# Performance work log

Hardware: AMD Instinct MI355X
Metric: run time of the kernel (lower is better)

## Reference

```python
import jax, jax.numpy as jnp
import numpy as np

B, N, D = 4, 1024, 1024
H, DH = 16, 64            # heads, dim_head; inner_dim = H*DH = D
CTX_N, CTX_D = 77, 768    # CLIP text context
FF_IN, FF_HID = 8 * D, 4 * D  # GEGLU: proj to 2*4*D, gate to 4*D
EPS = 1e-5
SCALE = DH ** -0.5
NL = 256                  # 2**8 levels for all quantizers
ZP_QKV = 128.0            # asymmetric 8-bit zero point for q/k/v
ZP_W = 0.0                # always_zero=True for softmax-weight quantizer


def _round_ste(t):
    return t + jax.lax.stop_gradient(jnp.round(t) - t)


def _fake_quant(x, delta, zp):
    xq = jnp.clip(_round_ste(x / delta) + zp, 0.0, NL - 1.0)
    return (xq - zp) * delta


def _ln(x, w, b):
    m = x.mean(-1, keepdims=True)
    v = x.var(-1, keepdims=True)
    return (x - m) * jax.lax.rsqrt(v + EPS) * w + b


def _split_heads(t):  # [b, n, h*d] -> [b, h, n, d]
    b, n, _ = t.shape
    return t.reshape(b, n, H, DH).transpose(0, 2, 1, 3)


def _attn(x, ctx, wq, wk, wv, wo, bo, dq, dk, dv, dw):
    q = _split_heads(x @ wq)
    k = _split_heads(ctx @ wk)
    v = _split_heads(ctx @ wv)
    qq = _fake_quant(q, dq, ZP_QKV)
    kk = _fake_quant(k, dk, ZP_QKV)
    sim = jnp.einsum('bhid,bhjd->bhij', qq, kk) * SCALE
    attn = jax.nn.softmax(sim, axis=-1)
    aw = _fake_quant(attn, dw, ZP_W)
    vv = _fake_quant(v, dv, ZP_QKV)
    out = jnp.einsum('bhij,bhjd->bhid', aw, vv)
    b, _, n, _ = out.shape
    out = out.transpose(0, 2, 1, 3).reshape(b, n, H * DH)
    return out @ wo + bo


def _geglu_ff(x, w1, b1, w2, b2):
    h = x @ w1 + b1
    a, g = jnp.split(h, 2, axis=-1)
    return (a * jax.nn.gelu(g, approximate=False)) @ w2 + b2


def setup_inputs() -> dict:
    key = jax.random.key(0)
    ks = jax.random.split(key, 16)
    w = lambda i, shp, s: jax.random.normal(ks[i], shp, jnp.float32) * s
    sD = D ** -0.5
    sC = CTX_D ** -0.5
    return {
        'x': jax.random.normal(ks[0], (B, N, D), jnp.float32),
        'context': jax.random.normal(ks[1], (B, CTX_N, CTX_D), jnp.float32),
        'norm1_w': jnp.ones((D,), jnp.float32), 'norm1_b': jnp.zeros((D,), jnp.float32),
        'norm2_w': jnp.ones((D,), jnp.float32), 'norm2_b': jnp.zeros((D,), jnp.float32),
        'norm3_w': jnp.ones((D,), jnp.float32), 'norm3_b': jnp.zeros((D,), jnp.float32),
        'a1_wq': w(2, (D, D), sD), 'a1_wk': w(3, (D, D), sD), 'a1_wv': w(4, (D, D), sD),
        'a1_wo': w(5, (D, D), sD), 'a1_bo': jnp.zeros((D,), jnp.float32),
        'a2_wq': w(6, (D, D), sD), 'a2_wk': w(7, (CTX_D, D), sC), 'a2_wv': w(8, (CTX_D, D), sC),
        'a2_wo': w(9, (D, D), sD), 'a2_bo': jnp.zeros((D,), jnp.float32),
        'ff_w1': w(10, (D, FF_IN), sD), 'ff_b1': jnp.zeros((FF_IN,), jnp.float32),
        'ff_w2': w(11, (FF_HID, D), FF_HID ** -0.5), 'ff_b2': jnp.zeros((D,), jnp.float32),
        'd1_q': jnp.asarray(0.02, jnp.float32), 'd1_k': jnp.asarray(0.02, jnp.float32),
        'd1_v': jnp.asarray(0.02, jnp.float32), 'd1_w': jnp.asarray(1.0 / 255.0, jnp.float32),
        'd2_q': jnp.asarray(0.02, jnp.float32), 'd2_k': jnp.asarray(0.02, jnp.float32),
        'd2_v': jnp.asarray(0.02, jnp.float32), 'd2_w': jnp.asarray(1.0 / 255.0, jnp.float32),
    }


def reference(x, context, norm1_w, norm1_b, norm2_w, norm2_b, norm3_w, norm3_b,
              a1_wq, a1_wk, a1_wv, a1_wo, a1_bo,
              a2_wq, a2_wk, a2_wv, a2_wo, a2_bo,
              ff_w1, ff_b1, ff_w2, ff_b2,
              d1_q, d1_k, d1_v, d1_w, d2_q, d2_k, d2_v, d2_w):
    # attn1: quantized self-attention
    x = _attn(_ln(x, norm1_w, norm1_b), _ln(x, norm1_w, norm1_b),
              a1_wq, a1_wk, a1_wv, a1_wo, a1_bo, d1_q, d1_k, d1_v, d1_w) + x
    # attn2: quantized cross-attention with text context
    x = _attn(_ln(x, norm2_w, norm2_b), context,
              a2_wq, a2_wk, a2_wv, a2_wo, a2_bo, d2_q, d2_k, d2_v, d2_w) + x
    # GEGLU feed-forward
    x = _geglu_ff(_ln(x, norm3_w, norm3_b), ff_w1, ff_b1, ff_w2, ff_b2) + x
    return x
```

## Files before the change

### kernel.cpp

```cpp
#include <hip/hip_runtime.h>
#include <math.h>


typedef unsigned short u16;
typedef __attribute__((ext_vector_type(8))) short short8;
typedef __attribute__((ext_vector_type(4))) float f32x4;

__device__ inline float b2f(u16 v) { return __uint_as_float(((unsigned)v) << 16); }
__device__ inline u16 f2b(float f) {
  unsigned u = __float_as_uint(f);
  unsigned r = u + 0x7fffu + ((u >> 16) & 1u);
  return (u16)(r >> 16);
}

__device__ inline void glds16(const u16* g, u16* l) {
  __builtin_amdgcn_global_load_lds(
      (const __attribute__((address_space(1))) void*)g,
      (__attribute__((address_space(3))) void*)l, 16, 0, 0);
}

__global__ __launch_bounds__(256) void transpose_k(const float* __restrict__ in,
                                                   u16* __restrict__ out,
                                                   int R, int C) {
  __shared__ float t[32][33];
  int tx = threadIdx.x & 31, ty = threadIdx.x >> 5;
  int c0 = blockIdx.x * 32, r0 = blockIdx.y * 32;
#pragma unroll
  for (int i = 0; i < 32; i += 8)
    t[ty + i][tx] = in[(size_t)(r0 + ty + i) * C + c0 + tx];
  __syncthreads();
#pragma unroll
  for (int i = 0; i < 32; i += 8)
    out[(size_t)(c0 + ty + i) * R + r0 + tx] = f2b(t[tx][ty + i]);
}

__global__ __launch_bounds__(256) void tr16_k(const u16* __restrict__ in,
                                              u16* __restrict__ out, int NK,
                                              int NKP) {
  __shared__ u16 t[32][33];
  int tx = threadIdx.x & 31, ty = threadIdx.x >> 5;
  int n0 = blockIdx.x * 32, c0 = blockIdx.y * 32, b = blockIdx.z;
  const u16* ib = in + (size_t)b * NK * 1024;
  u16* ob = out + (size_t)b * 1024 * NKP;
#pragma unroll
  for (int i = 0; i < 32; i += 8) {
    int n = n0 + ty + i;
    n = n < NK ? n : NK - 1;
    t[ty + i][tx] = ib[(size_t)n * 1024 + c0 + tx];
  }
  __syncthreads();
#pragma unroll
  for (int i = 0; i < 32; i += 8)
    ob[(size_t)(c0 + ty + i) * NKP + n0 + tx] = t[tx][ty + i];
}

__global__ __launch_bounds__(256) void cast_k(const float* __restrict__ in,
                                              u16* __restrict__ out) {
  int i = (blockIdx.x * 256 + threadIdx.x) * 4;
  float4 v = *(const float4*)(in + i);
  out[i + 0] = f2b(v.x);
  out[i + 1] = f2b(v.y);
  out[i + 2] = f2b(v.z);
  out[i + 3] = f2b(v.w);
}

__global__ __launch_bounds__(256) void ln_k(const float* __restrict__ X,
                                            const float* __restrict__ W,
                                            const float* __restrict__ Bi,
                                            u16* __restrict__ Out) {
  const int row = blockIdx.x, tid = threadIdx.x;
  float4 x = *(const float4*)(X + (size_t)row * 1024 + tid * 4);
  float s = x.x + x.y + x.z + x.w;
  float s2 = x.x * x.x + x.y * x.y + x.z * x.z + x.w * x.w;
#pragma unroll
  for (int off = 32; off >= 1; off >>= 1) {
    s += __shfl_down(s, off);
    s2 += __shfl_down(s2, off);
  }
  __shared__ float red[8];
  int wave = tid >> 6, lane = tid & 63;
  if (lane == 0) { red[wave] = s; red[4 + wave] = s2; }
  __syncthreads();
  s = red[0] + red[1] + red[2] + red[3];
  s2 = red[4] + red[5] + red[6] + red[7];
  float mean = s * 0.0009765625f;
  float var = s2 * 0.0009765625f - mean * mean;
  float rs = rsqrtf(var + 1e-5f);
  float4 w = *(const float4*)(W + tid * 4);
  float4 b = *(const float4*)(Bi + tid * 4);
  u16* orow = Out + (size_t)row * 1024 + tid * 4;
  orow[0] = f2b((x.x - mean) * rs * w.x + b.x);
  orow[1] = f2b((x.y - mean) * rs * w.y + b.y);
  orow[2] = f2b((x.z - mean) * rs * w.z + b.z);
  orow[3] = f2b((x.w - mean) * rs * w.w + b.w);
}

template <int EPI>
__global__ __launch_bounds__(256, 2) void gemm_bt(
    const u16* __restrict__ A, int lda, const u16* __restrict__ Bt, int ldb,
    void* __restrict__ Cp, int ldc, const float* __restrict__ bias,
    const float* __restrict__ res, int ldr, const float* __restrict__ dp,
    int M, int N, int K) {
  __shared__ __align__(16) u16 As[128 * 64];
  __shared__ __align__(16) u16 Bs[128 * 64];
  const int tid = threadIdx.x;
  const int lane = tid & 63, wave = tid >> 6;
  const int qd = lane >> 4, cl = lane & 15;
  const int wm = (wave & 1) << 6, wn = (wave >> 1) << 6;
  const int m0 = blockIdx.x * 128, n0 = blockIdx.y * 128;

  f32x4 acc[4][4];
  const f32x4 zero = {0.f, 0.f, 0.f, 0.f};
#pragma unroll
  for (int i = 0; i < 4; i++)
#pragma unroll
    for (int j = 0; j < 4; j++) acc[i][j] = zero;

  for (int k0 = 0; k0 < K; k0 += 64) {
    __syncthreads();
#pragma unroll
    for (int it = 0; it < 4; ++it) {
      int ch = it * 256 + tid;
      int r = ch >> 3, cc = (ch & 7) << 3;
      int gr = m0 + r;
      gr = gr < M ? gr : M - 1;
      glds16(A + (size_t)gr * lda + k0 + cc, As + ch * 8);
      glds16(Bt + (size_t)(n0 + r) * ldb + k0 + cc, Bs + ch * 8);
    }
    __syncthreads();
#pragma unroll
    for (int ks = 0; ks < 64; ks += 32) {
      short8 af[4], bf[4];
#pragma unroll
      for (int t = 0; t < 4; t++)
        af[t] = *(const short8*)(As + (wm + t * 16 + cl) * 64 + ks + qd * 8);
#pragma unroll
      for (int t = 0; t < 4; t++)
        bf[t] = *(const short8*)(Bs + (wn + t * 16 + cl) * 64 + ks + qd * 8);
#pragma unroll
      for (int mt = 0; mt < 4; mt++)
#pragma unroll
        for (int nt = 0; nt < 4; nt++)
          acc[mt][nt] = __builtin_amdgcn_mfma_f32_16x16x32_bf16(
              af[mt], bf[nt], acc[mt][nt], 0, 0, 0);
    }
  }

  float dscale = 1.f;
  if constexpr (EPI == 0) dscale = 1.0f / dp[0];
#pragma unroll
  for (int mt = 0; mt < 4; ++mt) {
#pragma unroll
    for (int r = 0; r < 4; ++r) {
      int row = m0 + wm + mt * 16 + qd * 4 + r;
      if (row >= M) continue;
#pragma unroll
      for (int nt = 0; nt < 4; ++nt) {
        int col = n0 + wn + nt * 16 + cl;
        float v = acc[mt][nt][r];
        if constexpr (EPI == 0) {
          float xq = rintf(v * dscale) + 128.f;
          xq = fminf(fmaxf(xq, 0.f), 255.f);
          ((u16*)Cp)[(size_t)row * ldc + col] = f2b(xq - 128.f);
        } else {
          v += bias[col] + res[(size_t)row * ldr + col];
          ((float*)Cp)[(size_t)row * ldc + col] = v;
        }
      }
    }
  }
}

__global__ __launch_bounds__(256, 2) void ff1_geglu_k(
    const u16* __restrict__ A, const u16* __restrict__ W1t,
    const float* __restrict__ b1, u16* __restrict__ gg, int M) {
  __shared__ __align__(16) u16 As[128 * 64];
  __shared__ __align__(16) u16 Ba[64 * 64];
  __shared__ __align__(16) u16 Bg[64 * 64];
  const int tid = threadIdx.x;
  const int lane = tid & 63, wave = tid >> 6;
  const int qd = lane >> 4, cl = lane & 15;
  const int wm = (wave & 1) << 6, wn = (wave >> 1) << 5;
  const int m0 = blockIdx.x * 128, n0 = blockIdx.y * 64;

  f32x4 aca[4][2], acg[4][2];
  const f32x4 zero = {0.f, 0.f, 0.f, 0.f};
#pragma unroll
  for (int i = 0; i < 4; i++)
#pragma unroll
    for (int j = 0; j < 2; j++) { aca[i][j] = zero; acg[i][j] = zero; }

  for (int k0 = 0; k0 < 1024; k0 += 64) {
    __syncthreads();
#pragma unroll
    for (int it = 0; it < 4; ++it) {
      int ch = it * 256 + tid;
      int r = ch >> 3, cc = (ch & 7) << 3;
      glds16(A + (size_t)(m0 + r) * 1024 + k0 + cc, As + ch * 8);
    }
#pragma unroll
    for (int it = 0; it < 2; ++it) {
      int ch = it * 256 + tid;
      int r = ch >> 3, cc = (ch & 7) << 3;
      glds16(W1t + (size_t)(n0 + r) * 1024 + k0 + cc, Ba + ch * 8);
      glds16(W1t + (size_t)(4096 + n0 + r) * 1024 + k0 + cc, Bg + ch * 8);
    }
    __syncthreads();
#pragma unroll
    for (int ks = 0; ks < 64; ks += 32) {
      short8 af[4], ba[2], bg[2];
#pragma unroll
      for (int t = 0; t < 4; t++)
        af[t] = *(const short8*)(As + (wm + t * 16 + cl) * 64 + ks + qd * 8);
#pragma unroll
      for (int t = 0; t < 2; t++) {
        ba[t] = *(const short8*)(Ba + (wn + t * 16 + cl) * 64 + ks + qd * 8);
        bg[t] = *(const short8*)(Bg + (wn + t * 16 + cl) * 64 + ks + qd * 8);
      }
#pragma unroll
      for (int mt = 0; mt < 4; mt++)
#pragma unroll
        for (int nt = 0; nt < 2; nt++) {
          aca[mt][nt] = __builtin_amdgcn_mfma_f32_16x16x32_bf16(
              af[mt], ba[nt], aca[mt][nt], 0, 0, 0);
          acg[mt][nt] = __builtin_amdgcn_mfma_f32_16x16x32_bf16(
              af[mt], bg[nt], acg[mt][nt], 0, 0, 0);
        }
    }
  }
#pragma unroll
  for (int mt = 0; mt < 4; ++mt)
#pragma unroll
    for (int r = 0; r < 4; ++r) {
      int row = m0 + wm + mt * 16 + qd * 4 + r;
#pragma unroll
      for (int nt = 0; nt < 2; ++nt) {
        int col = n0 + wn + nt * 16 + cl;
        float a = aca[mt][nt][r] + b1[col];
        float g = acg[mt][nt][r] + b1[4096 + col];
        float ge = 0.5f * g * (1.0f + erff(g * 0.70710678118654752f));
        gg[(size_t)row * 4096 + col] = f2b(a * ge);
      }
    }
}

__global__ __launch_bounds__(256, 4) void attn_k(
    const u16* __restrict__ Q, const u16* __restrict__ Kb,
    const u16* __restrict__ VbT, u16* __restrict__ O,
    const float* dqp, const float* dkp, const float* dvp, const float* dwp,
    int NK, int NKP) {
  __shared__ __align__(16) u16 Ks[64 * 64];
  __shared__ __align__(16) u16 VTs[64 * 64];
  __shared__ __align__(16) u16 Ps[4][16 * 72];
  const int tid = threadIdx.x;
  const int lane = tid & 63, wave = tid >> 6;
  const int qd = lane >> 4, cl = lane & 15;
  const int b = blockIdx.z, h = blockIdx.y, qt = blockIdx.x;
  const float sscale = dqp[0] * dkp[0] * 0.125f;
  const float oscale = dwp[0] * dvp[0];
  const float inv_dw = 1.0f / dwp[0];
  const f32x4 zero = {0.f, 0.f, 0.f, 0.f};

  const u16* qrow =
      Q + (size_t)(b * 1024 + qt * 64 + wave * 16 + cl) * 1024 + h * 64;
  short8 qf[2];
  qf[0] = *(const short8*)(qrow + qd * 8);
  qf[1] = *(const short8*)(qrow + 32 + qd * 8);

  const u16* kbase = Kb + (size_t)(b * NK) * 1024 + h * 64;
  const u16* vtbase = VbT + ((size_t)b * 1024 + h * 64) * NKP;
  const int r_st = tid >> 3, c_st = (tid & 7) << 3;

  float m_s = -1e30f, l_s = 0.f;
  for (int j0 = 0; j0 < NK; j0 += 64) {
    __syncthreads();
#pragma unroll
    for (int it = 0; it < 2; ++it) {
      int r = it * 32 + r_st;
      int j = j0 + r;
      j = j < NK ? j : NK - 1;
      glds16(kbase + (size_t)j * 1024 + c_st, Ks + (it * 256 + tid) * 8);
    }
    __syncthreads();
    const bool full = (j0 + 64 <= NK);
    float sc[16];
#pragma unroll
    for (int nt = 0; nt < 4; ++nt) {
      short8 kf0 = *(const short8*)(Ks + (nt * 16 + cl) * 64 + qd * 8);
      short8 kf1 = *(const short8*)(Ks + (nt * 16 + cl) * 64 + 32 + qd * 8);
      f32x4 st = zero;
      st = __builtin_amdgcn_mfma_f32_16x16x32_bf16(kf0, qf[0], st, 0, 0, 0);
      st = __builtin_amdgcn_mfma_f32_16x16x32_bf16(kf1, qf[1], st, 0, 0, 0);
#pragma unroll
      for (int r = 0; r < 4; ++r) {
        int key = j0 + nt * 16 + qd * 4 + r;
        sc[nt * 4 + r] = (full || key < NK) ? st[r] * sscale : -1e30f;
      }
    }
    float mx = sc[0];
#pragma unroll
    for (int i = 1; i < 16; ++i) mx = fmaxf(mx, sc[i]);
    mx = fmaxf(mx, __shfl_xor(mx, 16));
    mx = fmaxf(mx, __shfl_xor(mx, 32));
    float mn = fmaxf(m_s, mx);
    float ss = 0.f;
#pragma unroll
    for (int i = 0; i < 16; ++i) ss += __expf(sc[i] - mn);
    ss += __shfl_xor(ss, 16);
    ss += __shfl_xor(ss, 32);
    l_s = l_s * __expf(m_s - mn) + ss;
    m_s = mn;
  }
  const float m_q = m_s, il_q = 1.0f / l_s;

  f32x4 oacc[4];
#pragma unroll
  for (int t = 0; t < 4; t++) oacc[t] = zero;

  for (int j0 = 0; j0 < NK; j0 += 64) {
    __syncthreads();
#pragma unroll
    for (int it = 0; it < 2; ++it) {
      int r = it * 32 + r_st;
      int j = j0 + r;
      j = j < NK ? j : NK - 1;
      glds16(kbase + (size_t)j * 1024 + c_st, Ks + (it * 256 + tid) * 8);
      glds16(vtbase + (size_t)r * NKP + j0 + c_st, VTs + (it * 256 + tid) * 8);
    }
    __syncthreads();
    const bool full = (j0 + 64 <= NK);
#pragma unroll
    for (int nt = 0; nt < 4; ++nt) {
      short8 kf0 = *(const short8*)(Ks + (nt * 16 + cl) * 64 + qd * 8);
      short8 kf1 = *(const short8*)(Ks + (nt * 16 + cl) * 64 + 32 + qd * 8);
      f32x4 st = zero;
      st = __builtin_amdgcn_mfma_f32_16x16x32_bf16(kf0, qf[0], st, 0, 0, 0);
      st = __builtin_amdgcn_mfma_f32_16x16x32_bf16(kf1, qf[1], st, 0, 0, 0);
      u16 pk[4];
#pragma unroll
      for (int r = 0; r < 4; ++r) {
        int key = j0 + nt * 16 + qd * 4 + r;
        float aw = 0.f;
        if (full || key < NK) {
          float attn = __expf(st[r] * sscale - m_q) * il_q;
          aw = fminf(fmaxf(rintf(attn * inv_dw), 0.f), 255.f);
        }
        pk[r] = f2b(aw);
      }
      uint2 pv;
      pv.x = (unsigned)pk[0] | ((unsigned)pk[1] << 16);
      pv.y = (unsigned)pk[2] | ((unsigned)pk[3] << 16);
      *(uint2*)(&Ps[wave][cl * 72 + nt * 16 + qd * 4]) = pv;
    }
#pragma unroll
    for (int ks = 0; ks < 2; ++ks) {
      short8 pf = *(const short8*)(&Ps[wave][cl * 72 + ks * 32 + qd * 8]);
#pragma unroll
      for (int dt = 0; dt < 4; ++dt) {
        short8 vf =
            *(const short8*)(VTs + (dt * 16 + cl) * 64 + ks * 32 + qd * 8);
        oacc[dt] =
            __builtin_amdgcn_mfma_f32_16x16x32_bf16(pf, vf, oacc[dt], 0, 0, 0);
      }
    }
  }
#pragma unroll
  for (int dt = 0; dt < 4; ++dt)
#pragma unroll
    for (int r = 0; r < 4; r++) {
      size_t addr =
          (size_t)(b * 1024 + qt * 64 + wave * 16 + qd * 4 + r) * 1024 +
          h * 64 + dt * 16 + cl;
      O[addr] = f2b(oacc[dt][r] * oscale);
    }
}

extern "C" void kernel_launch(void* const* d_in, const int* in_sizes, int n_in,
                              void* d_out, int out_size, void* d_ws,
                              size_t ws_size, hipStream_t stream) {
  (void)in_sizes; (void)n_in; (void)out_size; (void)ws_size;
  const float* x    = (const float*)d_in[0];
  const float* ctx  = (const float*)d_in[1];
  const float* n1w  = (const float*)d_in[2];
  const float* n1b  = (const float*)d_in[3];
  const float* n2w  = (const float*)d_in[4];
  const float* n2b  = (const float*)d_in[5];
  const float* n3w  = (const float*)d_in[6];
  const float* n3b  = (const float*)d_in[7];
  const float* a1wq = (const float*)d_in[8];
  const float* a1wk = (const float*)d_in[9];
  const float* a1wv = (const float*)d_in[10];
  const float* a1wo = (const float*)d_in[11];
  const float* a1bo = (const float*)d_in[12];
  const float* a2wq = (const float*)d_in[13];
  const float* a2wk = (const float*)d_in[14];
  const float* a2wv = (const float*)d_in[15];
  const float* a2wo = (const float*)d_in[16];
  const float* a2bo = (const float*)d_in[17];
  const float* ffw1 = (const float*)d_in[18];
  const float* ffb1 = (const float*)d_in[19];
  const float* ffw2 = (const float*)d_in[20];
  const float* ffb2 = (const float*)d_in[21];
  const float* d1q = (const float*)d_in[22];
  const float* d1k = (const float*)d_in[23];
  const float* d1v = (const float*)d_in[24];
  const float* d1w = (const float*)d_in[25];
  const float* d2q = (const float*)d_in[26];
  const float* d2k = (const float*)d_in[27];
  const float* d2v = (const float*)d_in[28];
  const float* d2w = (const float*)d_in[29];

  char* ws = (char*)d_ws;
  const size_t MB = 1u << 20;
  u16* W    = (u16*)(ws + 0 * MB);
  u16* lnb  = (u16*)(ws + 16 * MB);
  u16* qb   = (u16*)(ws + 24 * MB);
  u16* kb   = (u16*)(ws + 32 * MB);
  u16* vb   = (u16*)(ws + 40 * MB);
  u16* vbT  = (u16*)(ws + 48 * MB);
  u16* ao   = (u16*)(ws + 56 * MB);
  float* x1 = (float*)(ws + 64 * MB);
  u16* k2b  = (u16*)(ws + 32 * MB);
  u16* v2b  = (u16*)(ws + 33 * MB);
  u16* vbTc = (u16*)(ws + 34 * MB);
  u16* ctxb = (u16*)(ws + 35 * MB);
  u16* gg   = (u16*)(ws + 24 * MB);

  u16* WT0 = W;
  u16* WT1 = (u16*)(ws + 2 * MB);
  u16* WT2 = (u16*)(ws + 4 * MB);
  u16* WT3 = (u16*)(ws + 6 * MB);

  dim3 T256(256);
  transpose_k<<<dim3(32, 32), T256, 0, stream>>>(a1wq, WT0, 1024, 1024);
  transpose_k<<<dim3(32, 32), T256, 0, stream>>>(a1wk, WT1, 1024, 1024);
  transpose_k<<<dim3(32, 32), T256, 0, stream>>>(a1wv, WT2, 1024, 1024);
  transpose_k<<<dim3(32, 32), T256, 0, stream>>>(a1wo, WT3, 1024, 1024);
  ln_k<<<4096, T256, 0, stream>>>(x, n1w, n1b, lnb);
  gemm_bt<0><<<dim3(32, 8), T256, 0, stream>>>(lnb, 1024, WT0, 1024, qb, 1024,
                                               nullptr, nullptr, 0, d1q, 4096,
                                               1024, 1024);
  gemm_bt<0><<<dim3(32, 8), T256, 0, stream>>>(lnb, 1024, WT1, 1024, kb, 1024,
                                               nullptr, nullptr, 0, d1k, 4096,
                                               1024, 1024);
  gemm_bt<0><<<dim3(32, 8), T256, 0, stream>>>(lnb, 1024, WT2, 1024, vb, 1024,
                                               nullptr, nullptr, 0, d1v, 4096,
                                               1024, 1024);
  tr16_k<<<dim3(32, 32, 4), T256, 0, stream>>>(vb, vbT, 1024, 1024);
  attn_k<<<dim3(16, 16, 4), T256, 0, stream>>>(qb, kb, vbT, ao, d1q, d1k, d1v,
                                               d1w, 1024, 1024);
  gemm_bt<1><<<dim3(32, 8), T256, 0, stream>>>(ao, 1024, WT3, 1024, x1, 1024,
                                               a1bo, x, 1024, nullptr, 4096,
                                               1024, 1024);
  transpose_k<<<dim3(32, 32), T256, 0, stream>>>(a2wq, WT0, 1024, 1024);
  transpose_k<<<dim3(32, 32), T256, 0, stream>>>(a2wo, WT1, 1024, 1024);
  transpose_k<<<dim3(32, 24), T256, 0, stream>>>(a2wk, WT2, 768, 1024);
  transpose_k<<<dim3(32, 24), T256, 0, stream>>>(a2wv, WT3, 768, 1024);
  ln_k<<<4096, T256, 0, stream>>>(x1, n2w, n2b, lnb);
  cast_k<<<231, T256, 0, stream>>>(ctx, ctxb);
  gemm_bt<0><<<dim3(32, 8), T256, 0, stream>>>(lnb, 1024, WT0, 1024, qb, 1024,
                                               nullptr, nullptr, 0, d2q, 4096,
                                               1024, 1024);
  gemm_bt<0><<<dim3(3, 8), T256, 0, stream>>>(ctxb, 768, WT2, 768, k2b, 1024,
                                              nullptr, nullptr, 0, d2k, 308,
                                              1024, 768);
  gemm_bt<0><<<dim3(3, 8), T256, 0, stream>>>(ctxb, 768, WT3, 768, v2b, 1024,
                                              nullptr, nullptr, 0, d2v, 308,
                                              1024, 768);
  tr16_k<<<dim3(3, 32, 4), T256, 0, stream>>>(v2b, vbTc, 77, 128);
  attn_k<<<dim3(16, 16, 4), T256, 0, stream>>>(qb, k2b, vbTc, ao, d2q, d2k,
                                               d2v, d2w, 77, 128);
  gemm_bt<1><<<dim3(32, 8), T256, 0, stream>>>(ao, 1024, WT1, 1024, x1, 1024,
                                               a2bo, x1, 1024, nullptr, 4096,
                                               1024, 1024);
  transpose_k<<<dim3(256, 32), T256, 0, stream>>>(ffw1, W, 1024, 8192);
  ln_k<<<4096, T256, 0, stream>>>(x1, n3w, n3b, lnb);
  ff1_geglu_k<<<dim3(32, 64), T256, 0, stream>>>(lnb, W, ffb1, gg, 4096);
  transpose_k<<<dim3(32, 128), T256, 0, stream>>>(ffw2, W, 4096, 1024);
  gemm_bt<1><<<dim3(32, 8), T256, 0, stream>>>(gg, 4096, W, 4096, d_out, 1024,
                                               ffb2, x1, 1024, nullptr, 4096,
                                               1024, 4096);
}
```

Measured before the change: 673.0 us.

## Fuse QKV projections, batch weight transposes, shrink GEMM tiles, two query groups per attention block

Fuses the separate Q/K/V (and cross-attention K/V) projection GEMMs into single launches, with a segmented quantizing epilogue that picks the per-segment scale and output buffer. Batches the four weight transposes into one launch. Adds a TM template parameter and uses 64-row tiles for the N=1024 GEMMs to get more blocks on the device. Makes each attention block handle 128 queries as two groups so the K/V tiles staged in shared memory are reused twice. Fewer launches and better occupancy and reuse are traded for higher register pressure in attention and smaller per-block reuse in the 64-row GEMMs.

```diff
diff --git a/kernel.cpp b/kernel.cpp
--- a/kernel.cpp
+++ b/kernel.cpp
@@ -28,6 +28,26 @@
 #pragma unroll
   for (int i = 0; i < 32; i += 8)
     t[ty + i][tx] = in[(size_t)(r0 + ty + i) * C + c0 + tx];
+  __syncthreads();
+#pragma unroll
+  for (int i = 0; i < 32; i += 8)
+    out[(size_t)(c0 + ty + i) * R + r0 + tx] = f2b(t[tx][ty + i]);
+}
+
+struct TrBatch { const float* in[4]; u16* out[4]; int R[4]; };
+__global__ __launch_bounds__(256) void transpose4_k(TrBatch a) {
+  int z = blockIdx.z;
+  const float* in = a.in[z];
+  u16* out = a.out[z];
+  int R = a.R[z];
+  int r0 = blockIdx.y * 32;
+  if (r0 >= R) return;
+  __shared__ float t[32][33];
+  int tx = threadIdx.x & 31, ty = threadIdx.x >> 5;
+  int c0 = blockIdx.x * 32;
+#pragma unroll
+  for (int i = 0; i < 32; i += 8)
+    t[ty + i][tx] = in[(size_t)(r0 + ty + i) * 1024 + c0 + tx];
   __syncthreads();
 #pragma unroll
   for (int i = 0; i < 32; i += 8)
@@ -95,50 +115,56 @@
   orow[3] = f2b((x.w - mean) * rs * w.w + b.w);
 }
 
-template <int EPI>
+template <int EPI, int TM>
 __global__ __launch_bounds__(256, 2) void gemm_bt(
     const u16* __restrict__ A, int lda, const u16* __restrict__ Bt, int ldb,
     void* __restrict__ Cp, int ldc, const float* __restrict__ bias,
     const float* __restrict__ res, int ldr, const float* __restrict__ dp,
-    int M, int N, int K) {
-  __shared__ __align__(16) u16 As[128 * 64];
+    const float* __restrict__ dp2, const float* __restrict__ dp3,
+    size_t segsz, int M, int N, int K) {
+  __shared__ __align__(16) u16 As[TM * 64];
   __shared__ __align__(16) u16 Bs[128 * 64];
   const int tid = threadIdx.x;
   const int lane = tid & 63, wave = tid >> 6;
   const int qd = lane >> 4, cl = lane & 15;
-  const int wm = (wave & 1) << 6, wn = (wave >> 1) << 6;
-  const int m0 = blockIdx.x * 128, n0 = blockIdx.y * 128;
-
-  f32x4 acc[4][4];
+  const int wm = (wave & 1) * (TM / 2), wn = (wave >> 1) << 6;
+  const int m0 = blockIdx.x * TM, n0 = blockIdx.y * 128;
+
+  f32x4 acc[TM / 32][4];
   const f32x4 zero = {0.f, 0.f, 0.f, 0.f};
 #pragma unroll
-  for (int i = 0; i < 4; i++)
+  for (int i = 0; i < TM / 32; i++)
 #pragma unroll
     for (int j = 0; j < 4; j++) acc[i][j] = zero;
 
   for (int k0 = 0; k0 < K; k0 += 64) {
     __syncthreads();
 #pragma unroll
-    for (int it = 0; it < 4; ++it) {
+    for (int it = 0; it < TM / 32; ++it) {
       int ch = it * 256 + tid;
       int r = ch >> 3, cc = (ch & 7) << 3;
       int gr = m0 + r;
       gr = gr < M ? gr : M - 1;
       glds16(A + (size_t)gr * lda + k0 + cc, As + ch * 8);
+    }
+#pragma unroll
+    for (int it = 0; it < 4; ++it) {
+      int ch = it * 256 + tid;
+      int r = ch >> 3, cc = (ch & 7) << 3;
       glds16(Bt + (size_t)(n0 + r) * ldb + k0 + cc, Bs + ch * 8);
     }
     __syncthreads();
 #pragma unroll
     for (int ks = 0; ks < 64; ks += 32) {
-      short8 af[4], bf[4];
-#pragma unroll
-      for (int t = 0; t < 4; t++)
+      short8 af[TM / 32], bf[4];
+#pragma unroll
+      for (int t = 0; t < TM / 32; t++)
         af[t] = *(const short8*)(As + (wm + t * 16 + cl) * 64 + ks + qd * 8);
 #pragma unroll
       for (int t = 0; t < 4; t++)
         bf[t] = *(const short8*)(Bs + (wn + t * 16 + cl) * 64 + ks + qd * 8);
 #pragma unroll
-      for (int mt = 0; mt < 4; mt++)
+      for (int mt = 0; mt < TM / 32; mt++)
 #pragma unroll
         for (int nt = 0; nt < 4; nt++)
           acc[mt][nt] = __builtin_amdgcn_mfma_f32_16x16x32_bf16(
@@ -147,9 +173,16 @@
   }
 
   float dscale = 1.f;
+  u16* qbase = (u16*)Cp;
   if constexpr (EPI == 0) dscale = 1.0f / dp[0];
-#pragma unroll
-  for (int mt = 0; mt < 4; ++mt) {
+  if constexpr (EPI == 2) {
+    int seg = n0 >> 10;
+    const float* ds = (seg == 0) ? dp : ((seg == 1) ? dp2 : dp3);
+    dscale = 1.0f / ds[0];
+    qbase = (u16*)Cp + (size_t)seg * segsz;
+  }
+#pragma unroll
+  for (int mt = 0; mt < TM / 32; ++mt) {
 #pragma unroll
     for (int r = 0; r < 4; ++r) {
       int row = m0 + wm + mt * 16 + qd * 4 + r;
@@ -161,7 +194,11 @@
         if constexpr (EPI == 0) {
           float xq = rintf(v * dscale) + 128.f;
           xq = fminf(fmaxf(xq, 0.f), 255.f);
-          ((u16*)Cp)[(size_t)row * ldc + col] = f2b(xq - 128.f);
+          qbase[(size_t)row * ldc + col] = f2b(xq - 128.f);
+        } else if constexpr (EPI == 2) {
+          float xq = rintf(v * dscale) + 128.f;
+          xq = fminf(fmaxf(xq, 0.f), 255.f);
+          qbase[(size_t)row * ldc + (col & 1023)] = f2b(xq - 128.f);
         } else {
           v += bias[col] + res[(size_t)row * ldr + col];
           ((float*)Cp)[(size_t)row * ldc + col] = v;
@@ -261,17 +298,21 @@
   const float inv_dw = 1.0f / dwp[0];
   const f32x4 zero = {0.f, 0.f, 0.f, 0.f};
 
-  const u16* qrow =
-      Q + (size_t)(b * 1024 + qt * 64 + wave * 16 + cl) * 1024 + h * 64;
-  short8 qf[2];
-  qf[0] = *(const short8*)(qrow + qd * 8);
-  qf[1] = *(const short8*)(qrow + 32 + qd * 8);
+  short8 qf[2][2];
+#pragma unroll
+  for (int g = 0; g < 2; ++g) {
+    const u16* qrow =
+        Q + (size_t)(b * 1024 + qt * 128 + g * 64 + wave * 16 + cl) * 1024 +
+        h * 64;
+    qf[g][0] = *(const short8*)(qrow + qd * 8);
+    qf[g][1] = *(const short8*)(qrow + 32 + qd * 8);
+  }
 
   const u16* kbase = Kb + (size_t)(b * NK) * 1024 + h * 64;
   const u16* vtbase = VbT + ((size_t)b * 1024 + h * 64) * NKP;
   const int r_st = tid >> 3, c_st = (tid & 7) << 3;
 
-  float m_s = -1e30f, l_s = 0.f;
+  float m_s[2] = {-1e30f, -1e30f}, l_s[2] = {0.f, 0.f};
   for (int j0 = 0; j0 < NK; j0 += 64) {
     __syncthreads();
 #pragma unroll
@@ -283,39 +324,44 @@
     }
     __syncthreads();
     const bool full = (j0 + 64 <= NK);
-    float sc[16];
-#pragma unroll
-    for (int nt = 0; nt < 4; ++nt) {
-      short8 kf0 = *(const short8*)(Ks + (nt * 16 + cl) * 64 + qd * 8);
-      short8 kf1 = *(const short8*)(Ks + (nt * 16 + cl) * 64 + 32 + qd * 8);
-      f32x4 st = zero;
-      st = __builtin_amdgcn_mfma_f32_16x16x32_bf16(kf0, qf[0], st, 0, 0, 0);
-      st = __builtin_amdgcn_mfma_f32_16x16x32_bf16(kf1, qf[1], st, 0, 0, 0);
-#pragma unroll
-      for (int r = 0; r < 4; ++r) {
-        int key = j0 + nt * 16 + qd * 4 + r;
-        sc[nt * 4 + r] = (full || key < NK) ? st[r] * sscale : -1e30f;
-      }
-    }
-    float mx = sc[0];
-#pragma unroll
-    for (int i = 1; i < 16; ++i) mx = fmaxf(mx, sc[i]);
-    mx = fmaxf(mx, __shfl_xor(mx, 16));
-    mx = fmaxf(mx, __shfl_xor(mx, 32));
-    float mn = fmaxf(m_s, mx);
-    float ss = 0.f;
-#pragma unroll
-    for (int i = 0; i < 16; ++i) ss += __expf(sc[i] - mn);
-    ss += __shfl_xor(ss, 16);
-    ss += __shfl_xor(ss, 32);
-    l_s = l_s * __expf(m_s - mn) + ss;
-    m_s = mn;
-  }
-  const float m_q = m_s, il_q = 1.0f / l_s;
-
-  f32x4 oacc[4];
-#pragma unroll
-  for (int t = 0; t < 4; t++) oacc[t] = zero;
+#pragma unroll
+    for (int g = 0; g < 2; ++g) {
+      float sc[16];
+#pragma unroll
+      for (int nt = 0; nt < 4; ++nt) {
+        short8 kf0 = *(const short8*)(Ks + (nt * 16 + cl) * 64 + qd * 8);
+        short8 kf1 = *(const short8*)(Ks + (nt * 16 + cl) * 64 + 32 + qd * 8);
+        f32x4 st = zero;
+        st = __builtin_amdgcn_mfma_f32_16x16x32_bf16(kf0, qf[g][0], st, 0, 0, 0);
+        st = __builtin_amdgcn_mfma_f32_16x16x32_bf16(kf1, qf[g][1], st, 0, 0, 0);
+#pragma unroll
+        for (int r = 0; r < 4; ++r) {
+          int key = j0 + nt * 16 + qd * 4 + r;
+          sc[nt * 4 + r] = (full || key < NK) ? st[r] * sscale : -1e30f;
+        }
+      }
+      float mx = sc[0];
+#pragma unroll
+      for (int i = 1; i < 16; ++i) mx = fmaxf(mx, sc[i]);
+      mx = fmaxf(mx, __shfl_xor(mx, 16));
+      mx = fmaxf(mx, __shfl_xor(mx, 32));
+      float mn = fmaxf(m_s[g], mx);
+      float ss = 0.f;
+#pragma unroll
+      for (int i = 0; i < 16; ++i) ss += __expf(sc[i] - mn);
+      ss += __shfl_xor(ss, 16);
+      ss += __shfl_xor(ss, 32);
+      l_s[g] = l_s[g] * __expf(m_s[g] - mn) + ss;
+      m_s[g] = mn;
+    }
+  }
+  float il_s[2] = {1.0f / l_s[0], 1.0f / l_s[1]};
+
+  f32x4 oacc[2][4];
+#pragma unroll
+  for (int g = 0; g < 2; ++g)
+#pragma unroll
+    for (int t = 0; t < 4; t++) oacc[g][t] = zero;
 
   for (int j0 = 0; j0 < NK; j0 += 64) {
     __syncthreads();
@@ -330,49 +376,54 @@
     __syncthreads();
     const bool full = (j0 + 64 <= NK);
 #pragma unroll
-    for (int nt = 0; nt < 4; ++nt) {
-      short8 kf0 = *(const short8*)(Ks + (nt * 16 + cl) * 64 + qd * 8);
-      short8 kf1 = *(const short8*)(Ks + (nt * 16 + cl) * 64 + 32 + qd * 8);
-      f32x4 st = zero;
-      st = __builtin_amdgcn_mfma_f32_16x16x32_bf16(kf0, qf[0], st, 0, 0, 0);
-      st = __builtin_amdgcn_mfma_f32_16x16x32_bf16(kf1, qf[1], st, 0, 0, 0);
-      u16 pk[4];
-#pragma unroll
-      for (int r = 0; r < 4; ++r) {
-        int key = j0 + nt * 16 + qd * 4 + r;
-        float aw = 0.f;
-        if (full || key < NK) {
-          float attn = __expf(st[r] * sscale - m_q) * il_q;
-          aw = fminf(fmaxf(rintf(attn * inv_dw), 0.f), 255.f);
+    for (int g = 0; g < 2; ++g) {
+#pragma unroll
+      for (int nt = 0; nt < 4; ++nt) {
+        short8 kf0 = *(const short8*)(Ks + (nt * 16 + cl) * 64 + qd * 8);
+        short8 kf1 = *(const short8*)(Ks + (nt * 16 + cl) * 64 + 32 + qd * 8);
+        f32x4 st = zero;
+        st = __builtin_amdgcn_mfma_f32_16x16x32_bf16(kf0, qf[g][0], st, 0, 0, 0);
+        st = __builtin_amdgcn_mfma_f32_16x16x32_bf16(kf1, qf[g][1], st, 0, 0, 0);
+        u16 pk[4];
+#pragma unroll
+        for (int r = 0; r < 4; ++r) {
+          int key = j0 + nt * 16 + qd * 4 + r;
+          float aw = 0.f;
+          if (full || key < NK) {
+            float attn = __expf(st[r] * sscale - m_s[g]) * il_s[g];
+            aw = fminf(fmaxf(rintf(attn * inv_dw), 0.f), 255.f);
+          }
+          pk[r] = f2b(aw);
         }
-        pk[r] = f2b(aw);
-      }
-      uint2 pv;
-      pv.x = (unsigned)pk[0] | ((unsigned)pk[1] << 16);
-      pv.y = (unsigned)pk[2] | ((unsigned)pk[3] << 16);
-      *(uint2*)(&Ps[wave][cl * 72 + nt * 16 + qd * 4]) = pv;
-    }
-#pragma unroll
-    for (int ks = 0; ks < 2; ++ks) {
-      short8 pf = *(const short8*)(&Ps[wave][cl * 72 + ks * 32 + qd * 8]);
-#pragma unroll
-      for (int dt = 0; dt < 4; ++dt) {
-        short8 vf =
-            *(const short8*)(VTs + (dt * 16 + cl) * 64 + ks * 32 + qd * 8);
-        oacc[dt] =
-            __builtin_amdgcn_mfma_f32_16x16x32_bf16(pf, vf, oacc[dt], 0, 0, 0);
-      }
-    }
-  }
-#pragma unroll
-  for (int dt = 0; dt < 4; ++dt)
-#pragma unroll
-    for (int r = 0; r < 4; r++) {
-      size_t addr =
-          (size_t)(b * 1024 + qt * 64 + wave * 16 + qd * 4 + r) * 1024 +
-          h * 64 + dt * 16 + cl;
-      O[addr] = f2b(oacc[dt][r] * oscale);
-    }
+        uint2 pv;
+        pv.x = (unsigned)pk[0] | ((unsigned)pk[1] << 16);
+        pv.y = (unsigned)pk[2] | ((unsigned)pk[3] << 16);
+        *(uint2*)(&Ps[wave][cl * 72 + nt * 16 + qd * 4]) = pv;
+      }
+#pragma unroll
+      for (int ks = 0; ks < 2; ++ks) {
+        short8 pf = *(const short8*)(&Ps[wave][cl * 72 + ks * 32 + qd * 8]);
+#pragma unroll
+        for (int dt = 0; dt < 4; ++dt) {
+          short8 vf =
+              *(const short8*)(VTs + (dt * 16 + cl) * 64 + ks * 32 + qd * 8);
+          oacc[g][dt] = __builtin_amdgcn_mfma_f32_16x16x32_bf16(
+              pf, vf, oacc[g][dt], 0, 0, 0);
+        }
+      }
+    }
+  }
+#pragma unroll
+  for (int g = 0; g < 2; ++g)
+#pragma unroll
+    for (int dt = 0; dt < 4; ++dt)
+#pragma unroll
+      for (int r = 0; r < 4; r++) {
+        size_t addr = (size_t)(b * 1024 + qt * 128 + g * 64 + wave * 16 +
+                               qd * 4 + r) * 1024 +
+                      h * 64 + dt * 16 + cl;
+        O[addr] = f2b(oacc[g][dt][r] * oscale);
+      }
 }
 
 extern "C" void kernel_launch(void* const* d_in, const int* in_sizes, int n_in,
@@ -421,7 +472,7 @@
   u16* ao   = (u16*)(ws + 56 * MB);
   float* x1 = (float*)(ws + 64 * MB);
   u16* k2b  = (u16*)(ws + 32 * MB);
-  u16* v2b  = (u16*)(ws + 33 * MB);
+  u16* v2b  = k2b + 308 * 1024;
   u16* vbTc = (u16*)(ws + 34 * MB);
   u16* ctxb = (u16*)(ws + 35 * MB);
   u16* gg   = (u16*)(ws + 24 * MB);
@@ -430,54 +481,54 @@
   u16* WT1 = (u16*)(ws + 2 * MB);
   u16* WT2 = (u16*)(ws + 4 * MB);
   u16* WT3 = (u16*)(ws + 6 * MB);
+  u16* WT3c = WT2 + 1024 * 768;
 
   dim3 T256(256);
-  transpose_k<<<dim3(32, 32), T256, 0, stream>>>(a1wq, WT0, 1024, 1024);
-  transpose_k<<<dim3(32, 32), T256, 0, stream>>>(a1wk, WT1, 1024, 1024);
-  transpose_k<<<dim3(32, 32), T256, 0, stream>>>(a1wv, WT2, 1024, 1024);
-  transpose_k<<<dim3(32, 32), T256, 0, stream>>>(a1wo, WT3, 1024, 1024);
+  {
+    TrBatch tb;
+    tb.in[0] = a1wq; tb.out[0] = WT0; tb.R[0] = 1024;
+    tb.in[1] = a1wk; tb.out[1] = WT1; tb.R[1] = 1024;
+    tb.in[2] = a1wv; tb.out[2] = WT2; tb.R[2] = 1024;
+    tb.in[3] = a1wo; tb.out[3] = WT3; tb.R[3] = 1024;
+    transpose4_k<<<dim3(32, 32, 4), T256, 0, stream>>>(tb);
+  }
   ln_k<<<4096, T256, 0, stream>>>(x, n1w, n1b, lnb);
-  gemm_bt<0><<<dim3(32, 8), T256, 0, stream>>>(lnb, 1024, WT0, 1024, qb, 1024,
-                                               nullptr, nullptr, 0, d1q, 4096,
-                                               1024, 1024);
-  gemm_bt<0><<<dim3(32, 8), T256, 0, stream>>>(lnb, 1024, WT1, 1024, kb, 1024,
-                                               nullptr, nullptr, 0, d1k, 4096,
-                                               1024, 1024);
-  gemm_bt<0><<<dim3(32, 8), T256, 0, stream>>>(lnb, 1024, WT2, 1024, vb, 1024,
-                                               nullptr, nullptr, 0, d1v, 4096,
-                                               1024, 1024);
+  gemm_bt<2, 128><<<dim3(32, 24), T256, 0, stream>>>(
+      lnb, 1024, WT0, 1024, qb, 1024, nullptr, nullptr, 0, d1q, d1k, d1v,
+      (size_t)4096 * 1024, 4096, 3072, 1024);
   tr16_k<<<dim3(32, 32, 4), T256, 0, stream>>>(vb, vbT, 1024, 1024);
-  attn_k<<<dim3(16, 16, 4), T256, 0, stream>>>(qb, kb, vbT, ao, d1q, d1k, d1v,
-                                               d1w, 1024, 1024);
-  gemm_bt<1><<<dim3(32, 8), T256, 0, stream>>>(ao, 1024, WT3, 1024, x1, 1024,
-                                               a1bo, x, 1024, nullptr, 4096,
-                                               1024, 1024);
-  transpose_k<<<dim3(32, 32), T256, 0, stream>>>(a2wq, WT0, 1024, 1024);
-  transpose_k<<<dim3(32, 32), T256, 0, stream>>>(a2wo, WT1, 1024, 1024);
-  transpose_k<<<dim3(32, 24), T256, 0, stream>>>(a2wk, WT2, 768, 1024);
-  transpose_k<<<dim3(32, 24), T256, 0, stream>>>(a2wv, WT3, 768, 1024);
+  attn_k<<<dim3(8, 16, 4), T256, 0, stream>>>(qb, kb, vbT, ao, d1q, d1k, d1v,
+                                              d1w, 1024, 1024);
+  gemm_bt<1, 64><<<dim3(64, 8), T256, 0, stream>>>(
+      ao, 1024, WT3, 1024, x1, 1024, a1bo, x, 1024, nullptr, nullptr, nullptr,
+      0, 4096, 1024, 1024);
+  {
+    TrBatch tb;
+    tb.in[0] = a2wq; tb.out[0] = WT0; tb.R[0] = 1024;
+    tb.in[1] = a2wo; tb.out[1] = WT1; tb.R[1] = 1024;
+    tb.in[2] = a2wk; tb.out[2] = WT2;  tb.R[2] = 768;
+    tb.in[3] = a2wv; tb.out[3] = WT3c; tb.R[3] = 768;
+    transpose4_k<<<dim3(32, 32, 4), T256, 0, stream>>>(tb);
+  }
   ln_k<<<4096, T256, 0, stream>>>(x1, n2w, n2b, lnb);
   cast_k<<<231, T256, 0, stream>>>(ctx, ctxb);
-  gemm_bt<0><<<dim3(32, 8), T256, 0, stream>>>(lnb, 1024, WT0, 1024, qb, 1024,
-                                               nullptr, nullptr, 0, d2q, 4096,
-                                               1024, 1024);
-  gemm_bt<0><<<dim3(3, 8), T256, 0, stream>>>(ctxb, 768, WT2, 768, k2b, 1024,
-                                              nullptr, nullptr, 0, d2k, 308,
-                                              1024, 768);
-  gemm_bt<0><<<dim3(3, 8), T256, 0, stream>>>(ctxb, 768, WT3, 768, v2b, 1024,
-                                              nullptr, nullptr, 0, d2v, 308,
-                                              1024, 768);
+  gemm_bt<0, 64><<<dim3(64, 8), T256, 0, stream>>>(
+      lnb, 1024, WT0, 1024, qb, 1024, nullptr, nullptr, 0, d2q, nullptr,
+      nullptr, 0, 4096, 1024, 1024);
+  gemm_bt<2, 64><<<dim3(5, 16), T256, 0, stream>>>(
+      ctxb, 768, WT2, 768, k2b, 1024, nullptr, nullptr, 0, d2k, d2v, nullptr,
+      (size_t)308 * 1024, 308, 2048, 768);
   tr16_k<<<dim3(3, 32, 4), T256, 0, stream>>>(v2b, vbTc, 77, 128);
-  attn_k<<<dim3(16, 16, 4), T256, 0, stream>>>(qb, k2b, vbTc, ao, d2q, d2k,
-                                               d2v, d2w, 77, 128);
-  gemm_bt<1><<<dim3(32, 8), T256, 0, stream>>>(ao, 1024, WT1, 1024, x1, 1024,
-                                               a2bo, x1, 1024, nullptr, 4096,
-                                               1024, 1024);
+  attn_k<<<dim3(8, 16, 4), T256, 0, stream>>>(qb, k2b, vbTc, ao, d2q, d2k, d2v,
+                                              d2w, 77, 128);
+  gemm_bt<1, 64><<<dim3(64, 8), T256, 0, stream>>>(
+      ao, 1024, WT1, 1024, x1, 1024, a2bo, x1, 1024, nullptr, nullptr, nullptr,
+      0, 4096, 1024, 1024);
   transpose_k<<<dim3(256, 32), T256, 0, stream>>>(ffw1, W, 1024, 8192);
   ln_k<<<4096, T256, 0, stream>>>(x1, n3w, n3b, lnb);
   ff1_geglu_k<<<dim3(32, 64), T256, 0, stream>>>(lnb, W, ffb1, gg, 4096);
   transpose_k<<<dim3(32, 128), T256, 0, stream>>>(ffw2, W, 4096, 1024);
-  gemm_bt<1><<<dim3(32, 8), T256, 0, stream>>>(gg, 4096, W, 4096, d_out, 1024,
-                                               ffb2, x1, 1024, nullptr, 4096,
-                                               1024, 4096);
-}
+  gemm_bt<1, 64><<<dim3(64, 8), T256, 0, stream>>>(
+      gg, 4096, W, 4096, d_out, 1024, ffb2, x1, 1024, nullptr, nullptr,
+      nullptr, 0, 4096, 1024, 4096);
+}
```

Result: faster. 588.6 us (-12.5%).
